# Optimization experiments

Measured on AMD Instinct MI355X. Metric: run time of the kernel, lower is better.

## Reference

```python
import jax, jax.numpy as jnp
import numpy as np

D_MODEL = 1024
N_HEADS = 16
D_FF = 4096
D_K = D_MODEL // N_HEADS


def _ln(x, g, b, eps=1e-5):
    mu = jnp.mean(x, axis=-1, keepdims=True)
    var = jnp.mean(jnp.square(x - mu), axis=-1, keepdims=True)
    return (x - mu) * jax.lax.rsqrt(var + eps) * g + b


def setup_inputs() -> dict:
    key = jax.random.key(0)
    ks = jax.random.split(key, 16)
    s = 0.02
    inp = {
        "x": jax.random.normal(ks[0], (2, 2048, D_MODEL), dtype=jnp.float32),
        "Wq": jax.random.normal(ks[1], (D_MODEL, D_MODEL), dtype=jnp.float32) * s,
        "bq": jnp.zeros((D_MODEL,), jnp.float32),
        "Wk": jax.random.normal(ks[2], (D_MODEL, D_MODEL), dtype=jnp.float32) * s,
        "bk": jnp.zeros((D_MODEL,), jnp.float32),
        "Wv": jax.random.normal(ks[3], (D_MODEL, D_MODEL), dtype=jnp.float32) * s,
        "bv": jnp.zeros((D_MODEL,), jnp.float32),
        "Wo": jax.random.normal(ks[4], (D_MODEL, D_MODEL), dtype=jnp.float32) * s,
        "bo": jnp.zeros((D_MODEL,), jnp.float32),
        "W1": jax.random.normal(ks[5], (D_MODEL, D_FF), dtype=jnp.float32) * s,
        "b1": jnp.zeros((D_FF,), jnp.float32),
        "W2": jax.random.normal(ks[6], (D_FF, D_MODEL), dtype=jnp.float32) * s,
        "b2": jnp.zeros((D_MODEL,), jnp.float32),
        "g1": jnp.ones((D_MODEL,), jnp.float32),
        "be1": jnp.zeros((D_MODEL,), jnp.float32),
        "g2": jnp.ones((D_MODEL,), jnp.float32),
        "be2": jnp.zeros((D_MODEL,), jnp.float32),
    }
    return inp


def reference(x, Wq, bq, Wk, bk, Wv, bv, Wo, bo, W1, b1, W2, b2, g1, be1, g2, be2):
    B, L, D = x.shape
    # QKV projections -> [B, H, L, d_k]
    q = (x @ Wq + bq).reshape(B, L, N_HEADS, D_K).transpose(0, 2, 1, 3)
    k = (x @ Wk + bk).reshape(B, L, N_HEADS, D_K).transpose(0, 2, 1, 3)
    v = (x @ Wv + bv).reshape(B, L, N_HEADS, D_K).transpose(0, 2, 1, 3)
    scores = jnp.einsum("bhqd,bhkd->bhqk", q, k) / jnp.sqrt(jnp.float32(D_K))
    attn = jax.nn.softmax(scores, axis=-1)
    ctx = jnp.einsum("bhqk,bhkd->bhqd", attn, v)
    ctx = ctx.transpose(0, 2, 1, 3).reshape(B, L, D)
    attn_out = ctx @ Wo + bo
    # residual + LN1
    h = _ln(x + attn_out, g1, be1)
    # FFN (exact GELU, matching torch F.gelu default)
    ff = jax.nn.gelu(h @ W1 + b1, approximate=False) @ W2 + b2
    return _ln(h + ff, g2, be2)
```

## Files before the change

### kernel.cpp

```cpp
#include <hip/hip_runtime.h>
#include <cmath>


typedef unsigned short u16;
typedef unsigned int u32;
typedef __attribute__((ext_vector_type(8))) __bf16 bf16x8;
typedef __attribute__((ext_vector_type(4))) float f32x4;

#define MFMA16(a, b, c) __builtin_amdgcn_mfma_f32_16x16x32_bf16(a, b, c, 0, 0, 0)

__device__ __forceinline__ u16 f2bf(float f) {
  u32 u = __builtin_bit_cast(u32, f);
  u += 0x7fffu + ((u >> 16) & 1u);
  return (u16)(u >> 16);
}

__device__ __forceinline__ u32 packtrunc(float lo, float hi) {
#if __has_builtin(__builtin_amdgcn_perm)
  return __builtin_amdgcn_perm(__builtin_bit_cast(u32, hi),
                               __builtin_bit_cast(u32, lo), 0x07060302u);
#else
  return (__builtin_bit_cast(u32, lo) >> 16) |
         (__builtin_bit_cast(u32, hi) & 0xFFFF0000u);
#endif
}

__device__ __forceinline__ bf16x8 ld_frag(const u16* p) {
  return __builtin_bit_cast(bf16x8, *(const uint4*)p);
}

__device__ __forceinline__ float fexp2(float x) {
#if __has_builtin(__builtin_amdgcn_exp2f)
  return __builtin_amdgcn_exp2f(x);
#else
  return exp2f(x);
#endif
}

__device__ __forceinline__ float frcp(float x) {
#if __has_builtin(__builtin_amdgcn_rcpf)
  return __builtin_amdgcn_rcpf(x);
#else
  return 1.0f / x;
#endif
}

__device__ __forceinline__ float gelu_f(float v) {
  float x = v * 0.70710678118654752f;
  float a = fabsf(x);
  float t = frcp(fmaf(0.3275911f, a, 1.0f));
  float p = fmaf(1.061405429f, t, -1.453152027f);
  p = fmaf(p, t, 1.421413741f);
  p = fmaf(p, t, -0.284496736f);
  p = fmaf(p, t, 0.254829592f);
  p = p * t;
  float e = fexp2(-a * a * 1.4426950408889634f);
  float er = copysignf(1.0f - p * e, x);
  return 0.5f * v * (1.0f + er);
}

__device__ __forceinline__ void gload16(const u16* g, u16* l) {
  __builtin_amdgcn_global_load_lds(
      (const __attribute__((address_space(1))) void*)g,
      (__attribute__((address_space(3))) void*)l, 16, 0, 0);
}

#define WAITVL(N) asm volatile("s_waitcnt vmcnt(" #N ") lgkmcnt(0)" ::: "memory")
#define BAR() do { __builtin_amdgcn_s_barrier(); asm volatile("" ::: "memory"); } while (0)

__global__ __launch_bounds__(256) void prep_k(
    const float* __restrict__ x,
    const float* __restrict__ Wq, const float* __restrict__ Wk,
    const float* __restrict__ Wv, const float* __restrict__ Wo,
    const float* __restrict__ W1, const float* __restrict__ W2,
    u16* __restrict__ xb, u16* __restrict__ wqkvT, u16* __restrict__ woT,
    u16* __restrict__ w1T, u16* __restrict__ w2T) {
  const int z = blockIdx.z;
  if (z >= 12) {
    long i = (((long)(z - 12) * 1024 + blockIdx.y * 32 + blockIdx.x) * 256 +
              threadIdx.x) * 4;
    float4 v = *(const float4*)(x + i);
    ushort4 o;
    o.x = f2bf(v.x); o.y = f2bf(v.y); o.z = f2bf(v.z); o.w = f2bf(v.w);
    *(ushort4*)(xb + i) = o;
    return;
  }
  __shared__ float tile[32][33];
  const float* src;
  u16* dst;
  int R, C, r0, c0;
  if (z < 4) {
    src = (z == 0) ? Wq : (z == 1) ? Wk : (z == 2) ? Wv : Wo;
    dst = (z < 3) ? (wqkvT + (size_t)z * 1024 * 1024) : woT;
    R = 1024; C = 1024;
    r0 = blockIdx.y * 32; c0 = blockIdx.x * 32;
  } else if (z < 8) {
    src = W1; dst = w1T; R = 1024; C = 4096;
    r0 = blockIdx.y * 32; c0 = (z - 4) * 1024 + blockIdx.x * 32;
  } else {
    src = W2; dst = w2T; R = 4096; C = 1024;
    r0 = (z - 8) * 1024 + blockIdx.y * 32; c0 = blockIdx.x * 32;
  }
  int tx = threadIdx.x & 31, ty = threadIdx.x >> 5;
#pragma unroll
  for (int i = 0; i < 4; i++)
    tile[ty + 8 * i][tx] = src[(long)(r0 + ty + 8 * i) * C + c0 + tx];
  __syncthreads();
#pragma unroll
  for (int i = 0; i < 4; i++)
    dst[(long)(c0 + ty + 8 * i) * R + r0 + tx] = f2bf(tile[tx][ty + 8 * i]);
}

template <int MODE>
__global__ __launch_bounds__(256, 3) void gemm128_k(
    const u16* __restrict__ A, const u16* __restrict__ BT,
    int N, int lda, int ldb, int Kc,
    const float* __restrict__ bias, float* __restrict__ outF,
    u16* __restrict__ outB, float* __restrict__ p1,
    u16* __restrict__ qd, u16* __restrict__ kd, u16* __restrict__ vTd,
    const float* __restrict__ bq, const float* __restrict__ bk,
    const float* __restrict__ bv) {
  __shared__ u16 As[3][128 * 32];
  __shared__ u16 Bs[3][128 * 32];
  const int tid = threadIdx.x;
  const int wave = tid >> 6, lane = tid & 63, quad = lane >> 4, l16 = lane & 15;
  const int wm = wave >> 1, wn = wave & 1;
  const int gx = gridDim.x;
  int flat = blockIdx.y * gx + blockIdx.x;
  const int cpx = (gx * gridDim.y) >> 3;
  flat = (flat & 7) * cpx + (flat >> 3);
  const int m0 = (flat / gx) * 128, n0 = (flat % gx) * 128;
  const int kz = blockIdx.z;
  const long kofs = (long)kz * Kc;
  const int KT = Kc >> 5;

  const int srow = lane >> 2;
  const int sseg = (lane & 3) ^ (srow & 3);
  const u16* aS = A + (long)(m0 + wave * 32 + srow) * lda + kofs + sseg * 8;
  const u16* bS = BT + (long)(n0 + wave * 32 + srow) * ldb + kofs + sseg * 8;

  auto stage = [&](int sb, int s) {
    const u16* pa = aS + (long)s * 32;
    gload16(pa, &As[sb][wave * 1024]);
    gload16(pa + 16 * (long)lda, &As[sb][wave * 1024 + 512]);
    const u16* pb = bS + (long)s * 32;
    gload16(pb, &Bs[sb][wave * 1024]);
    gload16(pb + 16 * (long)ldb, &Bs[sb][wave * 1024 + 512]);
  };

  int aro[4], bro[4];
#pragma unroll
  for (int f = 0; f < 4; f++) {
    int ra = wm * 64 + f * 16 + l16;
    aro[f] = ra * 32 + ((quad ^ (ra & 3)) * 8);
    int rb = wn * 64 + f * 16 + l16;
    bro[f] = rb * 32 + ((quad ^ (rb & 3)) * 8);
  }

  f32x4 acc[4][4] = {};

  stage(0, 0);
  stage(1, 1);
  int buf = 0;
#pragma unroll 1
  for (int t = 0; t < KT; ++t) {
    if (t < KT - 1) { WAITVL(4); } else { WAITVL(0); }
    BAR();
    bf16x8 af[4], bfr[4];
#pragma unroll
    for (int i = 0; i < 4; i++) af[i] = ld_frag(&As[buf][aro[i]]);
#pragma unroll
    for (int i = 0; i < 4; i++) bfr[i] = ld_frag(&Bs[buf][bro[i]]);
    if (t + 2 < KT) {
      int nb = buf + 2; if (nb >= 3) nb -= 3;
      stage(nb, t + 2);
    }
    __builtin_amdgcn_s_setprio(1);
#pragma unroll
    for (int mf = 0; mf < 4; mf++)
#pragma unroll
      for (int nf = 0; nf < 4; nf++)
        acc[mf][nf] = MFMA16(af[mf], bfr[nf], acc[mf][nf]);
    __builtin_amdgcn_s_setprio(0);
    if (++buf == 3) buf = 0;
  }

  if (MODE == 0) {
    const int nbase = n0 + wn * 64;
    const int mat = nbase >> 10;
    const float* bp = (mat == 0) ? bq : ((mat == 1) ? bk : bv);
    float bb[4];
    int hh0[4], dd0[4];
#pragma unroll
    for (int nf = 0; nf < 4; nf++) {
      int nn = (nbase + nf * 16 + l16) & 1023;
      bb[nf] = bp[nn];
      hh0[nf] = nn >> 6;
      dd0[nf] = nn & 63;
    }
    if (mat < 2) {
#pragma unroll
      for (int mf = 0; mf < 4; mf++) {
#pragma unroll
        for (int r = 0; r < 4; r++) {
          int mr = m0 + wm * 64 + mf * 16 + quad * 4 + r;
          int bI = mr >> 11, ll = mr & 2047;
#pragma unroll
          for (int nf = 0; nf < 4; nf++) {
            float v = acc[mf][nf][r] + bb[nf];
            long idx = ((long)((bI * 16 + hh0[nf]) * 2048 + ll)) * 64 + dd0[nf];
            if (mat == 0) {
              qd[idx] = f2bf(v * 0.18033688011112043f);
            } else {
              kd[idx] = f2bf(v);
            }
          }
        }
      }
    } else {
#pragma unroll
      for (int nf = 0; nf < 4; nf++) {
#pragma unroll
        for (int mf = 0; mf < 4; mf++) {
#pragma unroll
          for (int r = 0; r < 4; r++) {
            int mr = m0 + wm * 64 + mf * 16 + quad * 4 + r;
            int bI = mr >> 11, ll = mr & 2047;
            float v = acc[mf][nf][r] + bb[nf];
            vTd[((long)((bI * 16 + hh0[nf]) * 64 + dd0[nf])) * 2048 + ll] = f2bf(v);
          }
        }
      }
    }
  } else if (MODE == 2) {
    float bb[4];
#pragma unroll
    for (int nf = 0; nf < 4; nf++) bb[nf] = bias[n0 + wn * 64 + nf * 16 + l16];
#pragma unroll
    for (int mf = 0; mf < 4; mf++) {
#pragma unroll
      for (int r = 0; r < 4; r++) {
        int mr = m0 + wm * 64 + mf * 16 + quad * 4 + r;
        u16* orow = outB + (long)mr * N + n0 + wn * 64 + l16;
#pragma unroll
        for (int nf = 0; nf < 4; nf++)
          orow[nf * 16] = f2bf(gelu_f(acc[mf][nf][r] + bb[nf]));
      }
    }
  } else {
    float* sl = (kz == 0) ? outF : p1;
#pragma unroll
    for (int mf = 0; mf < 4; mf++) {
#pragma unroll
      for (int r = 0; r < 4; r++) {
        int mr = m0 + wm * 64 + mf * 16 + quad * 4 + r;
        float* orow = sl + (long)mr * N + n0 + wn * 64 + l16;
#pragma unroll
        for (int nf = 0; nf < 4; nf++) orow[nf * 16] = acc[mf][nf][r];
      }
    }
  }
}

__global__ __launch_bounds__(256, 3) void attn_k(const u16* __restrict__ qd,
                                                 const u16* __restrict__ kd,
                                                 const u16* __restrict__ vTd,
                                                 u16* __restrict__ ctx) {
  __shared__ u16 Ks[3][64 * 64];
  __shared__ u16 Vs[3][64 * 64];
  __shared__ __align__(16) u16 P[4][32][72];
  const int tid = threadIdx.x;
  const int wave = tid >> 6, lane = tid & 63, quad = lane >> 4, l16 = lane & 15;
  const int bh = blockIdx.y;
  const u16* Q = qd + (long)bh * 2048 * 64;
  const u16* Kp = kd + (long)bh * 2048 * 64;
  const u16* Vt = vTd + (long)bh * 64 * 2048;
  const int qbase = blockIdx.x * 128 + wave * 32;

  bf16x8 qf[2][2];
#pragma unroll
  for (int qs = 0; qs < 2; qs++) {
    qf[qs][0] = ld_frag(Q + (qbase + qs * 16 + l16) * 64 + quad * 8);
    qf[qs][1] = ld_frag(Q + (qbase + qs * 16 + l16) * 64 + 32 + quad * 8);
  }

  f32x4 o[2][4] = {};
  float m[2] = {-1e30f, -1e30f}, l[2] = {0.f, 0.f};

  const int srow = lane >> 3;
  const int sx = (lane & 7) ^ srow;
  const int kr0 = wave * 16 + srow;
  const int kr1 = wave * 16 + 8 + srow;

  const int fs0 = ((0 * 4 + quad) ^ (l16 & 7)) * 8;
  const int fs1 = ((1 * 4 + quad) ^ (l16 & 7)) * 8;

  auto stage = [&](int buf, int j0) {
    gload16(Kp + (long)(j0 + kr0) * 64 + sx * 8, &Ks[buf][(wave * 2 + 0) * 512]);
    gload16(Kp + (long)(j0 + kr1) * 64 + sx * 8, &Ks[buf][(wave * 2 + 1) * 512]);
    gload16(Vt + (long)kr0 * 2048 + j0 + sx * 8, &Vs[buf][(wave * 2 + 0) * 512]);
    gload16(Vt + (long)kr1 * 2048 + j0 + sx * 8, &Vs[buf][(wave * 2 + 1) * 512]);
  };

  stage(0, 0);
  stage(1, 64);
  int buf = 0;

#pragma unroll 1
  for (int j0 = 0; j0 < 2048; j0 += 64) {
    if (j0 < 2048 - 64) { WAITVL(4); } else { WAITVL(0); }
    BAR();
    if (j0 + 128 < 2048) {
      int nb = buf + 2; if (nb >= 3) nb -= 3;
      stage(nb, j0 + 128);
    }

    const u16* kb = &Ks[buf][0];
    f32x4 st[2][4];
#pragma unroll
    for (int f = 0; f < 4; f++) {
      bf16x8 k0 = ld_frag(kb + (f * 16 + l16) * 64 + fs0);
      bf16x8 k1 = ld_frag(kb + (f * 16 + l16) * 64 + fs1);
      f32x4 s0 = {}, s1 = {};
      s0 = MFMA16(k0, qf[0][0], s0); s0 = MFMA16(k1, qf[0][1], s0);
      s1 = MFMA16(k0, qf[1][0], s1); s1 = MFMA16(k1, qf[1][1], s1);
      st[0][f] = s0; st[1][f] = s1;
    }

#pragma unroll
    for (int qs = 0; qs < 2; qs++) {
      float mx = -1e30f;
#pragma unroll
      for (int f = 0; f < 4; f++)
        mx = fmaxf(mx, fmaxf(fmaxf(st[qs][f][0], st[qs][f][1]),
                             fmaxf(st[qs][f][2], st[qs][f][3])));
      mx = fmaxf(mx, __shfl_xor(mx, 16));
      mx = fmaxf(mx, __shfl_xor(mx, 32));
      if (__any(mx > m[qs] + 8.0f)) {
        float mn = fmaxf(m[qs], mx);
        float al = fexp2(m[qs] - mn);
        m[qs] = mn;
        l[qs] *= al;
#pragma unroll
        for (int nt = 0; nt < 4; nt++) {
          o[qs][nt][0] *= al; o[qs][nt][1] *= al;
          o[qs][nt][2] *= al; o[qs][nt][3] *= al;
        }
      }
      float sm = 0.f;
      u16* prow = &P[wave][qs * 16 + l16][0];
#pragma unroll
      for (int f = 0; f < 4; f++) {
        float p0 = fexp2(st[qs][f][0] - m[qs]);
        float p1 = fexp2(st[qs][f][1] - m[qs]);
        float p2 = fexp2(st[qs][f][2] - m[qs]);
        float p3 = fexp2(st[qs][f][3] - m[qs]);
        sm += (p0 + p1) + (p2 + p3);
        uint2 u;
        u.x = packtrunc(p0, p1);
        u.y = packtrunc(p2, p3);
        *(uint2*)(prow + f * 16 + quad * 4) = u;
      }
      sm += __shfl_xor(sm, 16);
      sm += __shfl_xor(sm, 32);
      l[qs] += sm;
    }
    __asm__ volatile("s_waitcnt lgkmcnt(0)" ::: "memory");

    const u16* vb = &Vs[buf][0];
    bf16x8 vf[4][2];
#pragma unroll
    for (int nt = 0; nt < 4; nt++) {
      vf[nt][0] = ld_frag(vb + (nt * 16 + l16) * 64 + fs0);
      vf[nt][1] = ld_frag(vb + (nt * 16 + l16) * 64 + fs1);
    }
#pragma unroll
    for (int qs = 0; qs < 2; qs++) {
      const u16* prow = &P[wave][qs * 16 + l16][0];
#pragma unroll
      for (int kh = 0; kh < 2; kh++) {
        bf16x8 pf = ld_frag(prow + kh * 32 + quad * 8);
#pragma unroll
        for (int nt = 0; nt < 4; nt++)
          o[qs][nt] = MFMA16(vf[nt][kh], pf, o[qs][nt]);
      }
    }
    if (++buf == 3) buf = 0;
  }

  const int bI = bh >> 4, hh = bh & 15;
#pragma unroll
  for (int qs = 0; qs < 2; qs++) {
    const float rl = 1.0f / l[qs];
    const long row = (long)(bI * 2048 + qbase + qs * 16 + l16);
#pragma unroll
    for (int nt = 0; nt < 4; nt++) {
      ushort4 w;
      w.x = f2bf(o[qs][nt][0] * rl);
      w.y = f2bf(o[qs][nt][1] * rl);
      w.z = f2bf(o[qs][nt][2] * rl);
      w.w = f2bf(o[qs][nt][3] * rl);
      *(ushort4*)(ctx + row * 1024 + hh * 64 + nt * 16 + quad * 4) = w;
    }
  }
}

__global__ __launch_bounds__(256) void ln2sb_k(const float* __restrict__ a,
                                               const float* __restrict__ q0,
                                               const float* __restrict__ q1,
                                               const float* __restrict__ bias,
                                               const float* __restrict__ g,
                                               const float* __restrict__ be,
                                               float* __restrict__ outF,
                                               u16* __restrict__ outB) {
  const int row = blockIdx.x, tid = threadIdx.x;
  const long base = (long)row * 1024;
  float v[4], s = 0.f, sq = 0.f;
#pragma unroll
  for (int i = 0; i < 4; i++) {
    int c = i * 256 + tid;
    float ff = q0[base + c] + q1[base + c] + bias[c];
    v[i] = a[base + c] + ff;
    s += v[i];
    sq += v[i] * v[i];
  }
#pragma unroll
  for (int off = 1; off < 64; off <<= 1) {
    s += __shfl_xor(s, off);
    sq += __shfl_xor(sq, off);
  }
  __shared__ float red[10];
  int wave = tid >> 6, lane = tid & 63;
  if (lane == 0) { red[wave * 2] = s; red[wave * 2 + 1] = sq; }
  __syncthreads();
  if (tid == 0) {
    float S = red[0] + red[2] + red[4] + red[6];
    float Q = red[1] + red[3] + red[5] + red[7];
    float mu = S * (1.0f / 1024.0f);
    float var = Q * (1.0f / 1024.0f) - mu * mu;
    red[8] = mu;
    red[9] = rsqrtf(var + 1e-5f);
  }
  __syncthreads();
  float mu = red[8], rstd = red[9];
#pragma unroll
  for (int i = 0; i < 4; i++) {
    int c = i * 256 + tid;
    float o = (v[i] - mu) * rstd * g[c] + be[c];
    outF[base + c] = o;
    if (outB) outB[base + c] = f2bf(o);
  }
}

extern "C" void kernel_launch(void* const* d_in, const int* in_sizes, int n_in,
                              void* d_out, int out_size, void* d_ws, size_t ws_size,
                              hipStream_t stream) {
  const float* x  = (const float*)d_in[0];
  const float* Wq = (const float*)d_in[1];  const float* bq = (const float*)d_in[2];
  const float* Wk = (const float*)d_in[3];  const float* bk = (const float*)d_in[4];
  const float* Wv = (const float*)d_in[5];  const float* bv = (const float*)d_in[6];
  const float* Wo = (const float*)d_in[7];  const float* bo = (const float*)d_in[8];
  const float* W1 = (const float*)d_in[9];  const float* b1 = (const float*)d_in[10];
  const float* W2 = (const float*)d_in[11]; const float* b2 = (const float*)d_in[12];
  const float* g1 = (const float*)d_in[13]; const float* be1 = (const float*)d_in[14];
  const float* g2 = (const float*)d_in[15]; const float* be2 = (const float*)d_in[16];

  char* ws = (char*)d_ws;
  size_t off = 0;
  auto alloc = [&](size_t bytes) {
    size_t o = off;
    off += (bytes + 255) & ~(size_t)255;
    return o;
  };
  u16*   xb     = (u16*)(ws + alloc(4096UL * 1024 * 2));
  u16*   wqkvT  = (u16*)(ws + alloc(3072UL * 1024 * 2));
  u16*   woT    = (u16*)(ws + alloc(1024UL * 1024 * 2));
  u16*   w1T    = (u16*)(ws + alloc(4096UL * 1024 * 2));
  u16*   w2T    = (u16*)(ws + alloc(1024UL * 4096 * 2));
  u16*   qb     = (u16*)(ws + alloc(32UL * 2048 * 64 * 2));
  u16*   kb     = (u16*)(ws + alloc(32UL * 2048 * 64 * 2));
  u16*   vTb    = (u16*)(ws + alloc(32UL * 64 * 2048 * 2));
  u16*   ctx    = (u16*)(ws + alloc(4096UL * 1024 * 2));
  float* attnO  = (float*)(ws + alloc(4096UL * 1024 * 4));
  float* h      = (float*)(ws + alloc(4096UL * 1024 * 4));
  u16*   hb     = (u16*)(ws + alloc(4096UL * 1024 * 2));
  u16*   ff1    = (u16*)(ws + alloc(4096UL * 4096 * 2));
  float* ff2    = (float*)(ws + alloc(4096UL * 1024 * 4));
  if (off > ws_size) return;

  float* wl0 = attnO;
  float* wl1 = ff2;
  float* sl0 = ff2;
  float* sl1 = attnO;

  prep_k<<<dim3(32, 32, 16), 256, 0, stream>>>(x, Wq, Wk, Wv, Wo, W1, W2,
                                               xb, wqkvT, woT, w1T, w2T);
  gemm128_k<0><<<dim3(24, 32), 256, 0, stream>>>(
      xb, wqkvT, 3072, 1024, 1024, 1024,
      nullptr, nullptr, nullptr, nullptr,
      qb, kb, vTb, bq, bk, bv);
  attn_k<<<dim3(16, 32), 256, 0, stream>>>(qb, kb, vTb, ctx);
  gemm128_k<3><<<dim3(8, 32, 2), 256, 0, stream>>>(
      ctx, woT, 1024, 1024, 1024, 512,
      nullptr, wl0, nullptr, wl1,
      nullptr, nullptr, nullptr, nullptr, nullptr, nullptr);
  ln2sb_k<<<4096, 256, 0, stream>>>(x, wl0, wl1, bo, g1, be1, h, hb);
  gemm128_k<2><<<dim3(32, 32), 256, 0, stream>>>(
      hb, w1T, 4096, 1024, 1024, 1024,
      b1, nullptr, ff1, nullptr,
      nullptr, nullptr, nullptr, nullptr, nullptr, nullptr);
  gemm128_k<3><<<dim3(8, 32, 2), 256, 0, stream>>>(
      ff1, w2T, 1024, 4096, 4096, 2048,
      nullptr, sl0, nullptr, sl1,
      nullptr, nullptr, nullptr, nullptr, nullptr, nullptr);
  ln2sb_k<<<4096, 256, 0, stream>>>(h, sl0, sl1, b2, g2, be2,
                                    (float*)d_out, nullptr);
}
```

Before: 371.7 us.

## Add 256x256 8-wave GEMM for QKV and FFN1, double-buffer attention

```diff
diff --git a/kernel.cpp b/kernel.cpp
--- a/kernel.cpp
+++ b/kernel.cpp
@@ -112,14 +112,173 @@
 }
 
 template <int MODE>
+__global__ __launch_bounds__(512, 2) void gemm256_8p(
+    const u16* __restrict__ A, const u16* __restrict__ BT,
+    int N, int lda, int ldb, int K,
+    const float* __restrict__ bias, u16* __restrict__ outB,
+    u16* __restrict__ qd, u16* __restrict__ kd, u16* __restrict__ vTd,
+    const float* __restrict__ bq, const float* __restrict__ bk,
+    const float* __restrict__ bv) {
+  __shared__ u16 As[2][2][128 * 64];
+  __shared__ u16 Bs[2][2][128 * 64];
+  const int tid = threadIdx.x;
+  const int wave = tid >> 6, lane = tid & 63, quad = lane >> 4, l16 = lane & 15;
+  const int wm = wave >> 2, wn = wave & 3;
+  const int gx = gridDim.x;
+  int flat = blockIdx.y * gx + blockIdx.x;
+  const int cpx = (gx * gridDim.y) >> 3;
+  flat = (flat & 7) * cpx + (flat >> 3);
+  const int m0 = (flat / gx) * 256, n0 = (flat % gx) * 256;
+  const int KT = K >> 6;
+
+  const int srow8 = lane >> 3;
+  const int sseg8 = (lane & 7) ^ srow8;
+  const u16* aSrc = A + (long)(m0 + wave * 8 + srow8) * lda + sseg8 * 8;
+  const u16* bSrc = BT + (long)(n0 + wave * 8 + srow8) * ldb + sseg8 * 8;
+
+  auto stageA = [&](int tt, int h) {
+    const u16* s = aSrc + (long)(h * 128) * lda + tt * 64;
+    u16* d = &As[tt & 1][h][wave * 512];
+    gload16(s, d);
+    gload16(s + 64 * (long)lda, d + 4096);
+  };
+  auto stageB = [&](int tt, int h) {
+    const u16* s = bSrc + (long)(h * 128) * ldb + tt * 64;
+    u16* d = &Bs[tt & 1][h][wave * 512];
+    gload16(s, d);
+    gload16(s + 64 * (long)ldb, d + 4096);
+  };
+
+  const int s7 = l16 & 7;
+  int lrB[4];
+#pragma unroll
+  for (int nf = 0; nf < 4; nf++) lrB[nf] = (wn & 1) * 64 + nf * 16 + l16;
+
+  f32x4 acc[8][4] = {};
+
+  stageA(0, 0); stageA(0, 1);
+  stageB(0, 0); stageB(0, 1);
+  stageA(1, 0); stageA(1, 1);
+  stageB(1, 0); stageB(1, 1);
+  WAITVL(8);
+  BAR();
+
+#pragma unroll 1
+  for (int t = 0; t < KT; ++t) {
+    const int buf = t & 1;
+    const u16* Ah = &As[buf][wm][0];
+    const u16* Bh = &Bs[buf][wn >> 1][0];
+    bf16x8 bfr[4][2];
+#pragma unroll
+    for (int q = 0; q < 4; ++q) {
+      if (q == 0) {
+#pragma unroll
+        for (int nf = 0; nf < 4; nf++)
+#pragma unroll
+          for (int kk = 0; kk < 2; kk++)
+            bfr[nf][kk] =
+                ld_frag(Bh + lrB[nf] * 64 + (((kk * 4 + quad) ^ s7) * 8));
+      }
+      bf16x8 af[2][2];
+#pragma unroll
+      for (int mfl = 0; mfl < 2; mfl++)
+#pragma unroll
+        for (int kk = 0; kk < 2; kk++)
+          af[mfl][kk] = ld_frag(Ah + (q * 32 + mfl * 16 + l16) * 64 +
+                                (((kk * 4 + quad) ^ s7) * 8));
+      if (q == 0) { if (t >= 1 && t + 1 < KT) stageA(t + 1, 0); }
+      else if (q == 1) { if (t >= 1 && t + 1 < KT) stageA(t + 1, 1); }
+      else if (q == 2) { if (t + 2 < KT) stageB(t + 2, 0); }
+      else {
+        if (t + 2 < KT) stageB(t + 2, 1);
+        if (t < KT - 2) { WAITVL(4); } else { WAITVL(0); }
+      }
+      BAR();
+      __builtin_amdgcn_s_setprio(1);
+#pragma unroll
+      for (int kk = 0; kk < 2; kk++)
+#pragma unroll
+        for (int mfl = 0; mfl < 2; mfl++)
+#pragma unroll
+          for (int nf = 0; nf < 4; nf++)
+            acc[q * 2 + mfl][nf] =
+                MFMA16(af[mfl][kk], bfr[nf][kk], acc[q * 2 + mfl][nf]);
+      __builtin_amdgcn_s_setprio(0);
+      BAR();
+    }
+  }
+
+  if (MODE == 0) {
+    const int nbase = n0 + wn * 64;
+    const int mat = nbase >> 10;
+    const float* bp = (mat == 0) ? bq : ((mat == 1) ? bk : bv);
+    float bb[4];
+    int hh0[4], dd0[4];
+#pragma unroll
+    for (int nf = 0; nf < 4; nf++) {
+      int nn = (nbase + nf * 16 + l16) & 1023;
+      bb[nf] = bp[nn];
+      hh0[nf] = nn >> 6;
+      dd0[nf] = nn & 63;
+    }
+    if (mat < 2) {
+#pragma unroll
+      for (int mf = 0; mf < 8; mf++) {
+#pragma unroll
+        for (int r = 0; r < 4; r++) {
+          int mr = m0 + wm * 128 + mf * 16 + quad * 4 + r;
+          int bI = mr >> 11, ll = mr & 2047;
+#pragma unroll
+          for (int nf = 0; nf < 4; nf++) {
+            float v = acc[mf][nf][r] + bb[nf];
+            long idx = ((long)((bI * 16 + hh0[nf]) * 2048 + ll)) * 64 + dd0[nf];
+            if (mat == 0) {
+              qd[idx] = f2bf(v * 0.18033688011112043f);
+            } else {
+              kd[idx] = f2bf(v);
+            }
+          }
+        }
+      }
+    } else {
+#pragma unroll
+      for (int nf = 0; nf < 4; nf++) {
+#pragma unroll
+        for (int mf = 0; mf < 8; mf++) {
+#pragma unroll
+          for (int r = 0; r < 4; r++) {
+            int mr = m0 + wm * 128 + mf * 16 + quad * 4 + r;
+            int bI = mr >> 11, ll = mr & 2047;
+            float v = acc[mf][nf][r] + bb[nf];
+            vTd[((long)((bI * 16 + hh0[nf]) * 64 + dd0[nf])) * 2048 + ll] = f2bf(v);
+          }
+        }
+      }
+    }
+  } else {
+    float bb[4];
+#pragma unroll
+    for (int nf = 0; nf < 4; nf++) bb[nf] = bias[n0 + wn * 64 + nf * 16 + l16];
+#pragma unroll
+    for (int mf = 0; mf < 8; mf++) {
+#pragma unroll
+      for (int r = 0; r < 4; r++) {
+        int mr = m0 + wm * 128 + mf * 16 + quad * 4 + r;
+        u16* orow = outB + (long)mr * N + n0 + wn * 64 + l16;
+#pragma unroll
+        for (int nf = 0; nf < 4; nf++)
+          orow[nf * 16] = f2bf(gelu_f(acc[mf][nf][r] + bb[nf]));
+      }
+    }
+  }
+}
+
+template <int MODE>
 __global__ __launch_bounds__(256, 3) void gemm128_k(
     const u16* __restrict__ A, const u16* __restrict__ BT,
     int N, int lda, int ldb, int Kc,
     const float* __restrict__ bias, float* __restrict__ outF,
-    u16* __restrict__ outB, float* __restrict__ p1,
-    u16* __restrict__ qd, u16* __restrict__ kd, u16* __restrict__ vTd,
-    const float* __restrict__ bq, const float* __restrict__ bk,
-    const float* __restrict__ bv) {
+    u16* __restrict__ outB, float* __restrict__ p1) {
   __shared__ u16 As[3][128 * 32];
   __shared__ u16 Bs[3][128 * 32];
   const int tid = threadIdx.x;
@@ -185,69 +344,7 @@
     if (++buf == 3) buf = 0;
   }
 
-  if (MODE == 0) {
-    const int nbase = n0 + wn * 64;
-    const int mat = nbase >> 10;
-    const float* bp = (mat == 0) ? bq : ((mat == 1) ? bk : bv);
-    float bb[4];
-    int hh0[4], dd0[4];
-#pragma unroll
-    for (int nf = 0; nf < 4; nf++) {
-      int nn = (nbase + nf * 16 + l16) & 1023;
-      bb[nf] = bp[nn];
-      hh0[nf] = nn >> 6;
-      dd0[nf] = nn & 63;
-    }
-    if (mat < 2) {
-#pragma unroll
-      for (int mf = 0; mf < 4; mf++) {
-#pragma unroll
-        for (int r = 0; r < 4; r++) {
-          int mr = m0 + wm * 64 + mf * 16 + quad * 4 + r;
-          int bI = mr >> 11, ll = mr & 2047;
-#pragma unroll
-          for (int nf = 0; nf < 4; nf++) {
-            float v = acc[mf][nf][r] + bb[nf];
-            long idx = ((long)((bI * 16 + hh0[nf]) * 2048 + ll)) * 64 + dd0[nf];
-            if (mat == 0) {
-              qd[idx] = f2bf(v * 0.18033688011112043f);
-            } else {
-              kd[idx] = f2bf(v);
-            }
-          }
-        }
-      }
-    } else {
-#pragma unroll
-      for (int nf = 0; nf < 4; nf++) {
-#pragma unroll
-        for (int mf = 0; mf < 4; mf++) {
-#pragma unroll
-          for (int r = 0; r < 4; r++) {
-            int mr = m0 + wm * 64 + mf * 16 + quad * 4 + r;
-            int bI = mr >> 11, ll = mr & 2047;
-            float v = acc[mf][nf][r] + bb[nf];
-            vTd[((long)((bI * 16 + hh0[nf]) * 64 + dd0[nf])) * 2048 + ll] = f2bf(v);
-          }
-        }
-      }
-    }
-  } else if (MODE == 2) {
-    float bb[4];
-#pragma unroll
-    for (int nf = 0; nf < 4; nf++) bb[nf] = bias[n0 + wn * 64 + nf * 16 + l16];
-#pragma unroll
-    for (int mf = 0; mf < 4; mf++) {
-#pragma unroll
-      for (int r = 0; r < 4; r++) {
-        int mr = m0 + wm * 64 + mf * 16 + quad * 4 + r;
-        u16* orow = outB + (long)mr * N + n0 + wn * 64 + l16;
-#pragma unroll
-        for (int nf = 0; nf < 4; nf++)
-          orow[nf * 16] = f2bf(gelu_f(acc[mf][nf][r] + bb[nf]));
-      }
-    }
-  } else {
+  {
     float* sl = (kz == 0) ? outF : p1;
 #pragma unroll
     for (int mf = 0; mf < 4; mf++) {
@@ -266,8 +363,8 @@
                                                  const u16* __restrict__ kd,
                                                  const u16* __restrict__ vTd,
                                                  u16* __restrict__ ctx) {
-  __shared__ u16 Ks[3][64 * 64];
-  __shared__ u16 Vs[3][64 * 64];
+  __shared__ u16 Ks[2][64 * 64];
+  __shared__ u16 Vs[2][64 * 64];
   __shared__ __align__(16) u16 P[4][32][72];
   const int tid = threadIdx.x;
   const int wave = tid >> 6, lane = tid & 63, quad = lane >> 4, l16 = lane & 15;
@@ -303,17 +400,12 @@
   };
 
   stage(0, 0);
-  stage(1, 64);
-  int buf = 0;
 
 #pragma unroll 1
   for (int j0 = 0; j0 < 2048; j0 += 64) {
-    if (j0 < 2048 - 64) { WAITVL(4); } else { WAITVL(0); }
-    BAR();
-    if (j0 + 128 < 2048) {
-      int nb = buf + 2; if (nb >= 3) nb -= 3;
-      stage(nb, j0 + 128);
-    }
+    const int buf = (j0 >> 6) & 1;
+    __syncthreads();
+    if (j0 + 64 < 2048) stage(buf ^ 1, j0 + 64);
 
     const u16* kb = &Ks[buf][0];
     f32x4 st[2][4];
@@ -385,7 +477,6 @@
           o[qs][nt] = MFMA16(vf[nt][kh], pf, o[qs][nt]);
       }
     }
-    if (++buf == 3) buf = 0;
   }
 
   const int bI = bh >> 4, hh = bh & 15;
@@ -495,24 +586,20 @@
 
   prep_k<<<dim3(32, 32, 16), 256, 0, stream>>>(x, Wq, Wk, Wv, Wo, W1, W2,
                                                xb, wqkvT, woT, w1T, w2T);
-  gemm128_k<0><<<dim3(24, 32), 256, 0, stream>>>(
+  gemm256_8p<0><<<dim3(12, 16), 512, 0, stream>>>(
       xb, wqkvT, 3072, 1024, 1024, 1024,
-      nullptr, nullptr, nullptr, nullptr,
-      qb, kb, vTb, bq, bk, bv);
+      nullptr, nullptr, qb, kb, vTb, bq, bk, bv);
   attn_k<<<dim3(16, 32), 256, 0, stream>>>(qb, kb, vTb, ctx);
   gemm128_k<3><<<dim3(8, 32, 2), 256, 0, stream>>>(
       ctx, woT, 1024, 1024, 1024, 512,
-      nullptr, wl0, nullptr, wl1,
-      nullptr, nullptr, nullptr, nullptr, nullptr, nullptr);
+      nullptr, wl0, nullptr, wl1);
   ln2sb_k<<<4096, 256, 0, stream>>>(x, wl0, wl1, bo, g1, be1, h, hb);
-  gemm128_k<2><<<dim3(32, 32), 256, 0, stream>>>(
+  gemm256_8p<2><<<dim3(16, 16), 512, 0, stream>>>(
       hb, w1T, 4096, 1024, 1024, 1024,
-      b1, nullptr, ff1, nullptr,
-      nullptr, nullptr, nullptr, nullptr, nullptr, nullptr);
+      b1, ff1, nullptr, nullptr, nullptr, nullptr, nullptr, nullptr);
   gemm128_k<3><<<dim3(8, 32, 2), 256, 0, stream>>>(
       ff1, w2T, 1024, 4096, 4096, 2048,
-      nullptr, sl0, nullptr, sl1,
-      nullptr, nullptr, nullptr, nullptr, nullptr, nullptr);
+      nullptr, sl0, nullptr, sl1);
   ln2sb_k<<<4096, 256, 0, stream>>>(h, sl0, sl1, b2, g2, be2,
                                     (float*)d_out, nullptr);
 }
```

New measurement: 356.5 us. 4.1% less time.
